# Kernel tuning notes

Hardware: AMD Instinct MI355X
Metric: run time of the kernel (lower is better)

## Reference

```python
import jax, jax.numpy as jnp
import numpy as np

N_NODES = 100000
N_EDGES = 1600000
F_IN, F_HID, F_OUT = 48, 16, 16
K = 2  # kernel_size, dim=1, degree=1 open B-spline -> basis (1-u, u)


def glorot(key, shape):
    fan_in, fan_out = shape[-2], shape[-1]
    s = jnp.sqrt(6.0 / (fan_in + fan_out))
    return jax.random.uniform(key, shape, jnp.float32, -s, s)


def setup_inputs() -> dict:
    key = jax.random.key(0)
    ks = jax.random.split(key, 10)
    x = jax.random.normal(ks[0], (N_NODES, F_IN), jnp.float32)
    edge_attr = jax.random.uniform(ks[1], (N_EDGES, 1), jnp.float32)
    edge_index = jax.random.randint(ks[2], (2, N_EDGES), 0, N_NODES, jnp.int64)
    W1 = glorot(ks[3], (K, F_IN, F_HID))
    root1 = glorot(ks[4], (F_IN, F_HID))
    b1 = jnp.zeros((F_HID,), jnp.float32)
    W2 = glorot(ks[5], (K, F_HID, F_OUT))
    root2 = glorot(ks[6], (F_HID, F_OUT))
    b2 = jnp.zeros((F_OUT,), jnp.float32)
    return {"x": x, "edge_attr": edge_attr, "edge_index": edge_index,
            "W1": W1, "root1": root1, "b1": b1, "W2": W2, "root2": root2, "b2": b2}


def spline_conv(x, edge_index, u, W, root, bias, num_nodes):
    # x: [N,Fin], u: [E] pseudo coords in [0,1], W: [2,Fin,Fout]
    src, dst = edge_index[0], edge_index[1]
    xj = x[src]                                        # [E,Fin] gather
    m = jnp.einsum('ef,kfo->eko', xj, W)               # [E,2,Fout]
    basis = jnp.stack([1.0 - u, u], axis=1)            # linear open B-spline, K=2
    msg = jnp.einsum('ek,eko->eo', basis, m)           # [E,Fout]
    agg = jax.ops.segment_sum(msg, dst, num_segments=num_nodes)
    cnt = jax.ops.segment_sum(jnp.ones_like(msg[:, 0]), dst, num_segments=num_nodes)
    agg = agg / jnp.maximum(cnt, 1.0)[:, None]         # aggr='mean'
    return agg + x @ root + bias                       # root_weight + bias


def reference(x, edge_attr, edge_index, W1, root1, b1, W2, root2, b2):
    u = edge_attr[:, 0]
    h = jax.nn.elu(spline_conv(x, edge_index, u, W1, root1, b1, N_NODES))
    out = spline_conv(h, edge_index, u, W2, root2, b2, N_NODES)
    return jax.nn.log_softmax(out, axis=1)
```

## Files before the change

### kernel.cpp

```cpp
#include <hip/hip_runtime.h>
#include <math.h>

#define N_NODES 100000
#define N_EDGES 1600000
#define KC 8
#define KSH 3
#define NBUK 391
#define NCHUNK 256
#define CPE 6250
#define M_CNT (NBUK * NCHUNK)
#define SCB 512
#define NSC ((M_CNT + SCB - 1) / SCB)

__device__ __forceinline__ unsigned bf16_rne(float x) {
    unsigned u = __float_as_uint(x);
    return (u + 0x7FFFu + ((u >> 16) & 1u)) >> 16;
}

__global__ __launch_bounds__(1024)
void fused_hist_transform(const float* __restrict__ X,
                          const float* __restrict__ W,
                          const float* __restrict__ root,
                          const float* __restrict__ bias,
                          unsigned* __restrict__ YPH, float* __restrict__ R,
                          const int* __restrict__ dst,
                          int* __restrict__ counts) {
    int t = threadIdx.x;
    if (blockIdx.x < NCHUNK) {
        __shared__ int h[NBUK];
        for (int i = t; i < NBUK; i += 1024) h[i] = 0;
        __syncthreads();
        int c = blockIdx.x;
        const int* dp = dst + c * CPE;
        for (int j = t; j < CPE; j += 1024) atomicAdd(&h[dp[j] >> 8], 1);
        __syncthreads();
        for (int i = t; i < NBUK; i += 1024) counts[i * NCHUNK + c] = h[i];
    } else {
        __shared__ float sW0[48 * 16];
        __shared__ float sWd[48 * 16];
        __shared__ float sR[48 * 16];
        __shared__ float sB[16];
        int bid = blockIdx.x - NCHUNK;
        for (int i = t; i < 48 * 16; i += 1024) {
            float w0 = W[i];
            float w1 = W[48 * 16 + i];
            sW0[i] = w0;
            sWd[i] = w1 - w0;
            sR[i]  = root[i];
        }
        if (t < 16) sB[t] = bias[t];
        __syncthreads();

        int idx = bid * 1024 + t;
        int n = idx >> 4;
        int o = idx & 15;
        if (n >= N_NODES) return;

        const float* xr = X + (long)n * 48;
        float a0 = 0.0f, a1 = 0.0f, ar = 0.0f;
        for (int f = 0; f < 48; ++f) {
            float xv = xr[f];
            a0 = fmaf(xv, sW0[f * 16 + o], a0);
            a1 = fmaf(xv, sWd[f * 16 + o], a1);
            ar = fmaf(xv, sR[f * 16 + o], ar);
        }
        YPH[idx] = bf16_rne(a0) | (bf16_rne(a1) << 16);
        R[idx]   = ar + sB[o];
    }
}

__global__ __launch_bounds__(SCB)
void scan_blocksum(const int* __restrict__ a, int* __restrict__ bsum) {
    __shared__ int s[SCB];
    int t = threadIdx.x;
    int i = blockIdx.x * SCB + t;
    s[t] = (i < M_CNT) ? a[i] : 0;
    __syncthreads();
    for (int off = SCB / 2; off > 0; off >>= 1) {
        if (t < off) s[t] += s[t + off];
        __syncthreads();
    }
    if (t == 0) bsum[blockIdx.x] = s[0];
}

__global__ __launch_bounds__(256)
void scan_bsum(int* __restrict__ bsum) {
    __shared__ int s[256];
    int t = threadIdx.x;
    int v = (t < NSC) ? bsum[t] : 0;
    s[t] = v;
    __syncthreads();
    for (int off = 1; off < 256; off <<= 1) {
        int x = (t >= off) ? s[t - off] : 0;
        __syncthreads();
        s[t] += x;
        __syncthreads();
    }
    if (t < NSC) bsum[t] = s[t] - v;
}

__global__ __launch_bounds__(SCB)
void scan_write(int* __restrict__ a, const int* __restrict__ bsum) {
    __shared__ int s[SCB];
    int t = threadIdx.x;
    int i = blockIdx.x * SCB + t;
    int v = (i < M_CNT) ? a[i] : 0;
    s[t] = v;
    __syncthreads();
    for (int off = 1; off < SCB; off <<= 1) {
        int x = (t >= off) ? s[t - off] : 0;
        __syncthreads();
        s[t] += x;
        __syncthreads();
    }
    if (i < M_CNT) a[i] = bsum[blockIdx.x] + s[t] - v;
}

__global__ __launch_bounds__(1024)
void scatter_edges(const int* __restrict__ src, const int* __restrict__ dst,
                   const float* __restrict__ u,
                   const int* __restrict__ offsets,
                   unsigned* __restrict__ pk, unsigned char* __restrict__ dl) {
    __shared__ unsigned upk[CPE];
    __shared__ unsigned short ubuk[CPE];
    __shared__ unsigned char udl[CPE];
    __shared__ unsigned spk[CPE];
    __shared__ unsigned char sdl[CPE];
    __shared__ int ls[NBUK + 1];
    __shared__ int lcur[NBUK];
    __shared__ int gbase[NBUK];
    __shared__ int sc[SCB];

    int t = threadIdx.x, c = blockIdx.x;

    for (int i = t; i < NBUK; i += 1024) lcur[i] = 0;
    __syncthreads();
    for (int j = t; j < CPE; j += 1024) {
        int e = c * CPE + j;
        int d = dst[e];
        float uu = u[e];
        uu = uu < 0.0f ? 0.0f : (uu > 1.0f ? 1.0f : uu);
        int u15 = (int)fmaf(uu, 32767.0f, 0.5f);
        upk[j] = (unsigned)src[e] | ((unsigned)u15 << 17);
        udl[j] = (unsigned char)(d & 255);
        int b = d >> 8;
        ubuk[j] = (unsigned short)b;
        atomicAdd(&lcur[b], 1);
    }
    __syncthreads();

    int v = 0;
    if (t < SCB) {
        v = (t < NBUK) ? lcur[t] : 0;
        sc[t] = v;
    }
    __syncthreads();
    for (int off = 1; off < SCB; off <<= 1) {
        int x = 0;
        if (t < SCB && t >= off) x = sc[t - off];
        __syncthreads();
        if (t < SCB) sc[t] += x;
        __syncthreads();
    }
    if (t < NBUK) {
        int ex = sc[t] - v;
        ls[t] = ex;
        lcur[t] = ex;
        gbase[t] = offsets[t * NCHUNK + c] - ex;
    }
    if (t == 0) ls[NBUK] = CPE;
    __syncthreads();

    for (int j = t; j < CPE; j += 1024) {
        int b = ubuk[j];
        int p = atomicAdd(&lcur[b], 1);
        spk[p] = upk[j];
        sdl[p] = udl[j];
    }
    __syncthreads();

    for (int j = t; j < CPE; j += 1024) {
        int lo = 0, hi = NBUK;
        while (hi - lo > 1) {
            int mid = (lo + hi) >> 1;
            if (ls[mid] <= j) lo = mid; else hi = mid;
        }
        int g = gbase[lo] + j;
        pk[g] = spk[j];
        dl[g] = sdl[j];
    }
}

__global__ __launch_bounds__(256)
void group_edges(const int* __restrict__ offsets,
                 const unsigned* __restrict__ pk_in,
                 const unsigned char* __restrict__ dl,
                 unsigned* __restrict__ pk_out,
                 int* __restrict__ rowptr) {
    __shared__ int h[256];
    __shared__ int pre[256];
    int b = blockIdx.x, t = threadIdx.x;
    int beg = offsets[b * NCHUNK];
    int end = (b + 1 < NBUK) ? offsets[(b + 1) * NCHUNK] : N_EDGES;
    h[t] = 0;
    __syncthreads();
    for (int j = beg + t; j < end; j += 256) atomicAdd(&h[dl[j]], 1);
    __syncthreads();
    int cntv = h[t];
    pre[t] = cntv;
    __syncthreads();
    for (int off = 1; off < 256; off <<= 1) {
        int x = (t >= off) ? pre[t - off] : 0;
        __syncthreads();
        pre[t] += x;
        __syncthreads();
    }
    int ex = pre[t] - cntv;
    int node0 = b << 8;
    if (node0 + t < N_NODES) rowptr[node0 + t] = beg + ex;
    if (b == 0 && t == 0) rowptr[N_NODES] = N_EDGES;
    __syncthreads();
    h[t] = ex;
    __syncthreads();
    for (int j = beg + t; j < end; j += 256) {
        int loc = dl[j];
        int pos = atomicAdd(&h[loc], 1);
        pk_out[beg + pos] = pk_in[j];
    }
}

__device__ __forceinline__ void octet_accumulate(
        int beg, int end, int h, const unsigned* __restrict__ csr,
        const unsigned* __restrict__ YPH, float* a0, float* a1) {
    float s0 = 0.0f, s1 = 0.0f;
    int j = beg;
    for (; j + 1 < end; j += 2) {
        unsigned p0 = csr[j];
        unsigned p1 = csr[j + 1];
        uint2 w0 = *(const uint2*)(YPH + (size_t)(p0 & 0x1FFFFu) * 16 + 2 * h);
        uint2 w1 = *(const uint2*)(YPH + (size_t)(p1 & 0x1FFFFu) * 16 + 2 * h);
        float u0 = (float)(p0 >> 17) * (1.0f / 32767.0f);
        float u1 = (float)(p1 >> 17) * (1.0f / 32767.0f);
        s0 += fmaf(u0, __uint_as_float(w0.x & 0xFFFF0000u), __uint_as_float(w0.x << 16));
        s1 += fmaf(u0, __uint_as_float(w0.y & 0xFFFF0000u), __uint_as_float(w0.y << 16));
        s0 += fmaf(u1, __uint_as_float(w1.x & 0xFFFF0000u), __uint_as_float(w1.x << 16));
        s1 += fmaf(u1, __uint_as_float(w1.y & 0xFFFF0000u), __uint_as_float(w1.y << 16));
    }
    if (j < end) {
        unsigned p0 = csr[j];
        uint2 w0 = *(const uint2*)(YPH + (size_t)(p0 & 0x1FFFFu) * 16 + 2 * h);
        float u0 = (float)(p0 >> 17) * (1.0f / 32767.0f);
        s0 += fmaf(u0, __uint_as_float(w0.x & 0xFFFF0000u), __uint_as_float(w0.x << 16));
        s1 += fmaf(u0, __uint_as_float(w0.y & 0xFFFF0000u), __uint_as_float(w0.y << 16));
    }
    *a0 = s0;
    *a1 = s1;
}

__global__ __launch_bounds__(256)
void aggregate_elu_transform(const int* __restrict__ rowptr,
                             const unsigned* __restrict__ csr,
                             const unsigned* __restrict__ YPH1,
                             const float* __restrict__ R1,
                             const float* __restrict__ W2,
                             const float* __restrict__ root2,
                             const float* __restrict__ b2,
                             unsigned* __restrict__ YPH2,
                             float* __restrict__ R2) {
    __shared__ float sW0[16 * 16];
    __shared__ float sWd[16 * 16];
    __shared__ float sR[16 * 16];
    __shared__ float sB[16];
    int t = threadIdx.x;
    {
        float w0 = W2[t];
        float w1 = W2[256 + t];
        sW0[t] = w0;
        sWd[t] = w1 - w0;
        sR[t]  = root2[t];
    }
    if (t < 16) sB[t] = b2[t];
    __syncthreads();

    int g = blockIdx.x * 256 + t;
    int n = g >> KSH;
    int h = g & (KC - 1);
    int beg = rowptr[n], end = rowptr[n + 1];
    int deg = end - beg;

    float a0, a1;
    octet_accumulate(beg, end, h, csr, YPH1, &a0, &a1);
    float inv = 1.0f / (deg > 0 ? (float)deg : 1.0f);

    float2 rr = ((const float2*)R1)[g];
    float v0 = fmaf(a0, inv, rr.x);
    float v1 = fmaf(a1, inv, rr.y);
    v0 = v0 > 0.0f ? v0 : expm1f(v0);
    v1 = v1 > 0.0f ? v1 : expm1f(v1);

    int base = (t & 63) & ~7;
    float h16[16];
#pragma unroll
    for (int k = 0; k < 8; ++k) {
        h16[2 * k + 0] = __shfl(v0, base + k, 64);
        h16[2 * k + 1] = __shfl(v1, base + k, 64);
    }

    int o0 = 2 * h;
    float y0 = 0.0f, y1 = 0.0f, yr = 0.0f;
    float z0 = 0.0f, z1 = 0.0f, zr = 0.0f;
#pragma unroll
    for (int f = 0; f < 16; ++f) {
        float hv = h16[f];
        y0 = fmaf(hv, sW0[f * 16 + o0], y0);
        y1 = fmaf(hv, sWd[f * 16 + o0], y1);
        yr = fmaf(hv, sR[f * 16 + o0],  yr);
        z0 = fmaf(hv, sW0[f * 16 + o0 + 1], z0);
        z1 = fmaf(hv, sWd[f * 16 + o0 + 1], z1);
        zr = fmaf(hv, sR[f * 16 + o0 + 1],  zr);
    }
    ((uint2*)YPH2)[g] = make_uint2(bf16_rne(y0) | (bf16_rne(y1) << 16),
                                   bf16_rne(z0) | (bf16_rne(z1) << 16));
    ((float2*)R2)[g] = make_float2(yr + sB[o0], zr + sB[o0 + 1]);
}

__global__ __launch_bounds__(256)
void aggregate_logsoftmax(const int* __restrict__ rowptr,
                          const unsigned* __restrict__ csr,
                          const unsigned* __restrict__ YPH,
                          const float* __restrict__ R,
                          float* __restrict__ out) {
    int g = blockIdx.x * 256 + threadIdx.x;
    int n = g >> KSH;
    int h = g & (KC - 1);
    int beg = rowptr[n], end = rowptr[n + 1];
    int deg = end - beg;

    float a0, a1;
    octet_accumulate(beg, end, h, csr, YPH, &a0, &a1);
    float inv = 1.0f / (deg > 0 ? (float)deg : 1.0f);

    float2 rr = ((const float2*)R)[g];
    float v0 = fmaf(a0, inv, rr.x);
    float v1 = fmaf(a1, inv, rr.y);

    float m = fmaxf(v0, v1);
#pragma unroll
    for (int mask = 1; mask <= 4; mask <<= 1) m = fmaxf(m, __shfl_xor(m, mask));
    float s = expf(v0 - m) + expf(v1 - m);
#pragma unroll
    for (int mask = 1; mask <= 4; mask <<= 1) s += __shfl_xor(s, mask);
    float lse = m + logf(s);

    ((float2*)out)[g] = make_float2(v0 - lse, v1 - lse);
}

extern "C" void kernel_launch(void* const* d_in, const int* in_sizes, int n_in,
                              void* d_out, int out_size, void* d_ws, size_t ws_size,
                              hipStream_t stream) {
    const float* x         = (const float*)d_in[0];
    const float* edge_attr = (const float*)d_in[1];
    const int*   edge_idx  = (const int*)d_in[2];
    const float* W1        = (const float*)d_in[3];
    const float* root1     = (const float*)d_in[4];
    const float* b1        = (const float*)d_in[5];
    const float* W2        = (const float*)d_in[6];
    const float* root2     = (const float*)d_in[7];
    const float* b2        = (const float*)d_in[8];
    float* out = (float*)d_out;

    const int* src = edge_idx;
    const int* dst = edge_idx + N_EDGES;

    char* ws = (char*)d_ws;
    unsigned*      pk_in   = (unsigned*)(ws);
    unsigned*      pk_out  = (unsigned*)(ws + 6400000);
    unsigned char* dl      = (unsigned char*)(ws + 12800000);
    int*           counts  = (int*)(ws + 14400000);
    int*           rowptr  = (int*)(ws + 14800384);
    unsigned*      YPH1    = (unsigned*)(ws + 15200400);
    unsigned*      YPH2    = (unsigned*)(ws + 21600400);
    float*         R1      = (float*)(ws + 28000400);
    float*         R2      = (float*)(ws + 34400400);
    int*           bsum    = (int*)(ws + 40800400);

    dim3 gK1(NCHUNK + (N_NODES * 16 + 1023) / 1024);
    dim3 gAgg((N_NODES * KC) / 256);

    fused_hist_transform<<<gK1, 1024, 0, stream>>>(
        x, W1, root1, b1, YPH1, R1, dst, counts);
    scan_blocksum<<<NSC, SCB, 0, stream>>>(counts, bsum);
    scan_bsum<<<1, 256, 0, stream>>>(bsum);
    scan_write<<<NSC, SCB, 0, stream>>>(counts, bsum);
    scatter_edges<<<NCHUNK, 1024, 0, stream>>>(src, dst, edge_attr,
                                               counts, pk_in, dl);
    group_edges<<<NBUK, 256, 0, stream>>>(counts, pk_in, dl, pk_out, rowptr);

    aggregate_elu_transform<<<gAgg, 256, 0, stream>>>(
        rowptr, pk_out, YPH1, R1, W2, root2, b2, YPH2, R2);

    aggregate_logsoftmax<<<gAgg, 256, 0, stream>>>(
        rowptr, pk_out, YPH2, R2, out);
}
```

Measured before the change: 216.9 us.

## Split packed node features into two half arrays for gather aggregation

The packed bf16 per-node table (16 words per node) is split into two separate 8-word arrays, one for each half of the output features. Each octet thread now gathers one 32-bit word per edge from each array in two passes instead of one 64-bit word, and the edge loop is unrolled by 4. The aim is a smaller per-node gather footprint per pass (32 bytes instead of 64), which should give better cache-line use and L2 locality. In exchange the CSR list is read twice and the output and R accesses are no longer vectorized.

```diff
diff --git a/kernel.cpp b/kernel.cpp
--- a/kernel.cpp
+++ b/kernel.cpp
@@ -22,7 +22,8 @@
                           const float* __restrict__ W,
                           const float* __restrict__ root,
                           const float* __restrict__ bias,
-                          unsigned* __restrict__ YPH, float* __restrict__ R,
+                          unsigned* __restrict__ YA, unsigned* __restrict__ YB,
+                          float* __restrict__ R,
                           const int* __restrict__ dst,
                           int* __restrict__ counts) {
     int t = threadIdx.x;
@@ -64,8 +65,10 @@
             a1 = fmaf(xv, sWd[f * 16 + o], a1);
             ar = fmaf(xv, sR[f * 16 + o], ar);
         }
-        YPH[idx] = bf16_rne(a0) | (bf16_rne(a1) << 16);
-        R[idx]   = ar + sB[o];
+        unsigned w = bf16_rne(a0) | (bf16_rne(a1) << 16);
+        if (o < 8) YA[n * 8 + o] = w;
+        else       YB[n * 8 + (o - 8)] = w;
+        R[idx] = ar + sB[o];
     }
 }
 
@@ -229,43 +232,46 @@
     }
 }
 
-__device__ __forceinline__ void octet_accumulate(
-        int beg, int end, int h, const unsigned* __restrict__ csr,
-        const unsigned* __restrict__ YPH, float* a0, float* a1) {
-    float s0 = 0.0f, s1 = 0.0f;
+__device__ __forceinline__ float half_accum(int beg, int end, int h,
+                                            const unsigned* __restrict__ csr,
+                                            const unsigned* __restrict__ Y) {
+    float acc = 0.0f;
     int j = beg;
-    for (; j + 1 < end; j += 2) {
-        unsigned p0 = csr[j];
-        unsigned p1 = csr[j + 1];
-        uint2 w0 = *(const uint2*)(YPH + (size_t)(p0 & 0x1FFFFu) * 16 + 2 * h);
-        uint2 w1 = *(const uint2*)(YPH + (size_t)(p1 & 0x1FFFFu) * 16 + 2 * h);
+    for (; j + 3 < end; j += 4) {
+        unsigned p0 = csr[j], p1 = csr[j + 1], p2 = csr[j + 2], p3 = csr[j + 3];
+        unsigned w0 = Y[(size_t)(p0 & 0x1FFFFu) * 8 + h];
+        unsigned w1 = Y[(size_t)(p1 & 0x1FFFFu) * 8 + h];
+        unsigned w2 = Y[(size_t)(p2 & 0x1FFFFu) * 8 + h];
+        unsigned w3 = Y[(size_t)(p3 & 0x1FFFFu) * 8 + h];
         float u0 = (float)(p0 >> 17) * (1.0f / 32767.0f);
         float u1 = (float)(p1 >> 17) * (1.0f / 32767.0f);
-        s0 += fmaf(u0, __uint_as_float(w0.x & 0xFFFF0000u), __uint_as_float(w0.x << 16));
-        s1 += fmaf(u0, __uint_as_float(w0.y & 0xFFFF0000u), __uint_as_float(w0.y << 16));
-        s0 += fmaf(u1, __uint_as_float(w1.x & 0xFFFF0000u), __uint_as_float(w1.x << 16));
-        s1 += fmaf(u1, __uint_as_float(w1.y & 0xFFFF0000u), __uint_as_float(w1.y << 16));
-    }
-    if (j < end) {
+        float u2 = (float)(p2 >> 17) * (1.0f / 32767.0f);
+        float u3 = (float)(p3 >> 17) * (1.0f / 32767.0f);
+        acc += fmaf(u0, __uint_as_float(w0 & 0xFFFF0000u), __uint_as_float(w0 << 16));
+        acc += fmaf(u1, __uint_as_float(w1 & 0xFFFF0000u), __uint_as_float(w1 << 16));
+        acc += fmaf(u2, __uint_as_float(w2 & 0xFFFF0000u), __uint_as_float(w2 << 16));
+        acc += fmaf(u3, __uint_as_float(w3 & 0xFFFF0000u), __uint_as_float(w3 << 16));
+    }
+    for (; j < end; ++j) {
         unsigned p0 = csr[j];
-        uint2 w0 = *(const uint2*)(YPH + (size_t)(p0 & 0x1FFFFu) * 16 + 2 * h);
+        unsigned w0 = Y[(size_t)(p0 & 0x1FFFFu) * 8 + h];
         float u0 = (float)(p0 >> 17) * (1.0f / 32767.0f);
-        s0 += fmaf(u0, __uint_as_float(w0.x & 0xFFFF0000u), __uint_as_float(w0.x << 16));
-        s1 += fmaf(u0, __uint_as_float(w0.y & 0xFFFF0000u), __uint_as_float(w0.y << 16));
-    }
-    *a0 = s0;
-    *a1 = s1;
+        acc += fmaf(u0, __uint_as_float(w0 & 0xFFFF0000u), __uint_as_float(w0 << 16));
+    }
+    return acc;
 }
 
 __global__ __launch_bounds__(256)
 void aggregate_elu_transform(const int* __restrict__ rowptr,
                              const unsigned* __restrict__ csr,
-                             const unsigned* __restrict__ YPH1,
+                             const unsigned* __restrict__ YA1,
+                             const unsigned* __restrict__ YB1,
                              const float* __restrict__ R1,
                              const float* __restrict__ W2,
                              const float* __restrict__ root2,
                              const float* __restrict__ b2,
-                             unsigned* __restrict__ YPH2,
+                             unsigned* __restrict__ YA2,
+                             unsigned* __restrict__ YB2,
                              float* __restrict__ R2) {
     __shared__ float sW0[16 * 16];
     __shared__ float sWd[16 * 16];
@@ -288,13 +294,12 @@
     int beg = rowptr[n], end = rowptr[n + 1];
     int deg = end - beg;
 
-    float a0, a1;
-    octet_accumulate(beg, end, h, csr, YPH1, &a0, &a1);
+    float sA = half_accum(beg, end, h, csr, YA1);
+    float sBv = half_accum(beg, end, h, csr, YB1);
     float inv = 1.0f / (deg > 0 ? (float)deg : 1.0f);
 
-    float2 rr = ((const float2*)R1)[g];
-    float v0 = fmaf(a0, inv, rr.x);
-    float v1 = fmaf(a1, inv, rr.y);
+    float v0 = fmaf(sA, inv, R1[n * 16 + h]);
+    float v1 = fmaf(sBv, inv, R1[n * 16 + 8 + h]);
     v0 = v0 > 0.0f ? v0 : expm1f(v0);
     v1 = v1 > 0.0f ? v1 : expm1f(v1);
 
@@ -302,32 +307,33 @@
     float h16[16];
 #pragma unroll
     for (int k = 0; k < 8; ++k) {
-        h16[2 * k + 0] = __shfl(v0, base + k, 64);
-        h16[2 * k + 1] = __shfl(v1, base + k, 64);
-    }
-
-    int o0 = 2 * h;
+        h16[k]     = __shfl(v0, base + k, 64);
+        h16[8 + k] = __shfl(v1, base + k, 64);
+    }
+
     float y0 = 0.0f, y1 = 0.0f, yr = 0.0f;
     float z0 = 0.0f, z1 = 0.0f, zr = 0.0f;
 #pragma unroll
     for (int f = 0; f < 16; ++f) {
         float hv = h16[f];
-        y0 = fmaf(hv, sW0[f * 16 + o0], y0);
-        y1 = fmaf(hv, sWd[f * 16 + o0], y1);
-        yr = fmaf(hv, sR[f * 16 + o0],  yr);
-        z0 = fmaf(hv, sW0[f * 16 + o0 + 1], z0);
-        z1 = fmaf(hv, sWd[f * 16 + o0 + 1], z1);
-        zr = fmaf(hv, sR[f * 16 + o0 + 1],  zr);
-    }
-    ((uint2*)YPH2)[g] = make_uint2(bf16_rne(y0) | (bf16_rne(y1) << 16),
-                                   bf16_rne(z0) | (bf16_rne(z1) << 16));
-    ((float2*)R2)[g] = make_float2(yr + sB[o0], zr + sB[o0 + 1]);
+        y0 = fmaf(hv, sW0[f * 16 + h], y0);
+        y1 = fmaf(hv, sWd[f * 16 + h], y1);
+        yr = fmaf(hv, sR[f * 16 + h],  yr);
+        z0 = fmaf(hv, sW0[f * 16 + 8 + h], z0);
+        z1 = fmaf(hv, sWd[f * 16 + 8 + h], z1);
+        zr = fmaf(hv, sR[f * 16 + 8 + h],  zr);
+    }
+    YA2[g] = bf16_rne(y0) | (bf16_rne(y1) << 16);
+    YB2[g] = bf16_rne(z0) | (bf16_rne(z1) << 16);
+    R2[n * 16 + h]     = yr + sB[h];
+    R2[n * 16 + 8 + h] = zr + sB[8 + h];
 }
 
 __global__ __launch_bounds__(256)
 void aggregate_logsoftmax(const int* __restrict__ rowptr,
                           const unsigned* __restrict__ csr,
-                          const unsigned* __restrict__ YPH,
+                          const unsigned* __restrict__ YA,
+                          const unsigned* __restrict__ YB,
                           const float* __restrict__ R,
                           float* __restrict__ out) {
     int g = blockIdx.x * 256 + threadIdx.x;
@@ -336,13 +342,12 @@
     int beg = rowptr[n], end = rowptr[n + 1];
     int deg = end - beg;
 
-    float a0, a1;
-    octet_accumulate(beg, end, h, csr, YPH, &a0, &a1);
+    float sA = half_accum(beg, end, h, csr, YA);
+    float sBv = half_accum(beg, end, h, csr, YB);
     float inv = 1.0f / (deg > 0 ? (float)deg : 1.0f);
 
-    float2 rr = ((const float2*)R)[g];
-    float v0 = fmaf(a0, inv, rr.x);
-    float v1 = fmaf(a1, inv, rr.y);
+    float v0 = fmaf(sA, inv, R[n * 16 + h]);
+    float v1 = fmaf(sBv, inv, R[n * 16 + 8 + h]);
 
     float m = fmaxf(v0, v1);
 #pragma unroll
@@ -352,7 +357,8 @@
     for (int mask = 1; mask <= 4; mask <<= 1) s += __shfl_xor(s, mask);
     float lse = m + logf(s);
 
-    ((float2*)out)[g] = make_float2(v0 - lse, v1 - lse);
+    out[n * 16 + h]     = v0 - lse;
+    out[n * 16 + 8 + h] = v1 - lse;
 }
 
 extern "C" void kernel_launch(void* const* d_in, const int* in_sizes, int n_in,
@@ -378,8 +384,10 @@
     unsigned char* dl      = (unsigned char*)(ws + 12800000);
     int*           counts  = (int*)(ws + 14400000);
     int*           rowptr  = (int*)(ws + 14800384);
-    unsigned*      YPH1    = (unsigned*)(ws + 15200400);
-    unsigned*      YPH2    = (unsigned*)(ws + 21600400);
+    unsigned*      YA1     = (unsigned*)(ws + 15200400);
+    unsigned*      YB1     = (unsigned*)(ws + 18400400);
+    unsigned*      YA2     = (unsigned*)(ws + 21600400);
+    unsigned*      YB2     = (unsigned*)(ws + 24800400);
     float*         R1      = (float*)(ws + 28000400);
     float*         R2      = (float*)(ws + 34400400);
     int*           bsum    = (int*)(ws + 40800400);
@@ -388,7 +396,7 @@
     dim3 gAgg((N_NODES * KC) / 256);
 
     fused_hist_transform<<<gK1, 1024, 0, stream>>>(
-        x, W1, root1, b1, YPH1, R1, dst, counts);
+        x, W1, root1, b1, YA1, YB1, R1, dst, counts);
     scan_blocksum<<<NSC, SCB, 0, stream>>>(counts, bsum);
     scan_bsum<<<1, 256, 0, stream>>>(bsum);
     scan_write<<<NSC, SCB, 0, stream>>>(counts, bsum);
@@ -397,8 +405,8 @@
     group_edges<<<NBUK, 256, 0, stream>>>(counts, pk_in, dl, pk_out, rowptr);
 
     aggregate_elu_transform<<<gAgg, 256, 0, stream>>>(
-        rowptr, pk_out, YPH1, R1, W2, root2, b2, YPH2, R2);
+        rowptr, pk_out, YA1, YB1, R1, W2, root2, b2, YA2, YB2, R2);
 
     aggregate_logsoftmax<<<gAgg, 256, 0, stream>>>(
-        rowptr, pk_out, YPH2, R2, out);
-}
+        rowptr, pk_out, YA2, YB2, R2, out);
+}
```

After: 220.6 us. No clear change (+1.7%).
